# Kernel optimization log

Measured on AMD Instinct MI355X. Metric: run time of the kernel, lower is better.

The kernel has to match this reference:

```python
import jax, jax.numpy as jnp
import numpy as np

EPS = 1e-7
TWO_PI = 2.0 * np.pi

K = 4096   # num gaussians
R = 8192   # num rays
MAP_SIZE = 100


def setup_inputs() -> dict:
    key = jax.random.key(0)
    k1, k2, k3, k4, k5, k6 = jax.random.split(key, 6)
    pos_raw = jax.random.normal(k1, (K, 2), dtype=jnp.float32)            # pre-sigmoid positions
    conc_raw = jax.random.normal(k2, (K,), dtype=jnp.float32)             # pre-softplus concentration
    scale_raw = 0.1 * jax.random.normal(k3, (K, 2), dtype=jnp.float32)    # log-scales
    rot_raw = jax.random.uniform(k4, (K,), dtype=jnp.float32) * TWO_PI    # rotation angles
    p_rays = jax.random.uniform(k5, (R, 2), dtype=jnp.float32) * MAP_SIZE # ray origins in map coords
    u = jax.random.normal(k6, (R, 2), dtype=jnp.float32)
    u_rays = u / jnp.linalg.norm(u, axis=-1, keepdims=True)               # unit ray directions
    return {"pos_raw": pos_raw, "conc_raw": conc_raw, "scale_raw": scale_raw,
            "rot_raw": rot_raw, "p_rays": p_rays, "u_rays": u_rays,
            "map_size": MAP_SIZE}


def _forward(pos_raw, conc_raw, scale_raw, rot_raw, p_rays, u_rays, map_size):
    # --- per-gaussian activations (GasSplattingModel getters) ---
    pos = jax.nn.sigmoid(pos_raw) * map_size           # (K,2)
    conc = jax.nn.softplus(conc_raw)                   # (K,)
    scale = jnp.exp(scale_raw)                         # (K,2)
    d0 = 1.0 / (scale[:, 0] ** 2 + EPS)                # diag of S^2 inverse
    d1 = 1.0 / (scale[:, 1] ** 2 + EPS)
    c, s = jnp.cos(rot_raw), jnp.sin(rot_raw)
    # Sigma^{-1} = R diag(d0,d1) R^T with R = [[c,-s],[s,c]]  (symmetric 2x2)
    m00 = c * c * d0 + s * s * d1                      # (K,)
    m01 = c * s * (d0 - d1)
    m11 = s * s * d0 + c * c * d1
    M = jnp.stack([m00, m01, m11], axis=0)             # (3,K) quadratic-form coeffs

    u0, u1 = u_rays[:, 0], u_rays[:, 1]
    p0, p1 = p_rays[:, 0], p_rays[:, 1]

    # quadratic-form features per ray, contracted with M via GEMM -> (R,K)
    qu = jnp.stack([u0 * u0, 2.0 * u0 * u1, u1 * u1], axis=1)        # (R,3)
    qp = jnp.stack([p0 * p0, 2.0 * p0 * p1, p1 * p1], axis=1)        # (R,3)
    qup = jnp.stack([u0 * p0, u0 * p1 + u1 * p0, u1 * p1], axis=1)   # (R,3)
    a = qu @ M          # u^T S u      (R,K)
    pSp = qp @ M        # p^T S p      (R,K)
    uSp = qup @ M       # u^T S p      (R,K)

    # S @ mu per gaussian -> (2,K)
    Sm = jnp.stack([m00 * pos[:, 0] + m01 * pos[:, 1],
                    m01 * pos[:, 0] + m11 * pos[:, 1]], axis=0)
    uSm = u_rays @ Sm   # u^T S mu     (R,K)
    pSm = p_rays @ Sm   # p^T S mu     (R,K)
    mSm = pos[:, 0] * Sm[0] + pos[:, 1] * Sm[1]        # mu^T S mu (K,)

    b = uSp - uSm                                      # u^T S (p - mu)
    c0 = pSp - 2.0 * pSm + mSm[None, :]                # (p-mu)^T S (p-mu)

    # closed-form line integral of conc * exp(-0.5 (x-mu)^T S (x-mu)) along ray
    dens = conc[None, :] * jnp.sqrt(TWO_PI / a) * jnp.exp(-0.5 * (c0 - b * b / a))
    return jnp.sum(dens, axis=-1)                      # (R,)


def reference(pos_raw, conc_raw, scale_raw, rot_raw, p_rays, u_rays, map_size):
    return _forward(pos_raw, conc_raw, scale_raw, rot_raw, p_rays, u_rays, map_size)
```

## Files before the change

### kernel.cpp

```cpp
#include <hip/hip_runtime.h>
#include <hip/hip_bf16.h>

#define EPS 1e-07f

#define BLOCK   512
#define RPB     32
#define SLICE_G 1024
#define NGRP    (SLICE_G/4)
#define NW      (BLOCK/64)
#define PBLOCK  64

#define SQRT_HALF_LOG2E 0.84932180028801904f
#define LOG2_SQRT_2PI   1.32574806473616588f

typedef float v4f __attribute__((ext_vector_type(4)));

__global__ __launch_bounds__(PBLOCK) void precompute_gauss(
                                 const float* __restrict__ pos_raw,
                                 const float* __restrict__ conc_raw,
                                 const float* __restrict__ scale_raw,
                                 const float* __restrict__ rot_raw,
                                 const void*  __restrict__ map_size_p,
                                 float* __restrict__ gG,
                                 float* __restrict__ out,
                                 int K, int KPAD, int R)
{
    int k = blockIdx.x * blockDim.x + threadIdx.x;
    int nthreads = gridDim.x * blockDim.x;

    for (int i = k; i < R; i += nthreads) out[i] = 0.0f;

    if (k >= KPAD) return;

    const int q = k >> 2, e = k & 3;
    float* rec = gG + q * 24;

    if (k >= K) {
        rec[0  + e] = 1.0f;
        rec[4  + e] = 0.0f;
        rec[8  + e] = 1.0f;
        rec[12 + e] = -1e38f;
        rec[16 + e] = 0.0f;
        rec[20 + e] = 0.0f;
        return;
    }

    unsigned int msbits = *(const unsigned int*)map_size_p;
    float msf = __uint_as_float(msbits);
    const float ms = (msf >= 1e-3f && msf <= 1e9f) ? msf
                                                   : (float)(*(const int*)map_size_p);

    float pr0 = pos_raw[2*k],  pr1 = pos_raw[2*k+1];
    float pos0 = ms / (1.0f + __expf(-pr0));
    float pos1 = ms / (1.0f + __expf(-pr1));

    float cr = conc_raw[k];
    float conc = fmaxf(cr, 0.0f) + __logf(1.0f + __expf(-fabsf(cr)));

    float s0 = __expf(scale_raw[2*k]);
    float s1 = __expf(scale_raw[2*k+1]);
    float d0 = 1.0f / (s0*s0 + EPS);
    float d1 = 1.0f / (s1*s1 + EPS);

    float rot = rot_raw[k];
    float c = __cosf(rot), s = __sinf(rot);

    float m00 = c*c*d0 + s*s*d1;
    float m01 = c*s*(d0 - d1);
    float m11 = s*s*d0 + c*c*d1;

    float det    = d0 * d1;
    float invdet = 1.0f / det;
    float cc = __log2f(conc) + LOG2_SQRT_2PI - 0.5f * __log2f(det);

    rec[0  + e] = m00 * invdet;
    rec[4  + e] = m01 * invdet;
    rec[8  + e] = m11 * invdet;
    rec[12 + e] = cc;
    rec[16 + e] = pos0;
    rec[20 + e] = pos1;
}

__global__ __launch_bounds__(BLOCK) void splat_main(
        const float* __restrict__ p_rays,
        const float* __restrict__ u_rays,
        const float* __restrict__ gG,
        float* __restrict__ out,
        int R)
{
    __shared__ v4f  sG4[NGRP * 6];
    __shared__ float psum[NW][RPB];

    const int tid   = threadIdx.x;
    const int lane  = tid & 63;
    const int wv    = tid >> 6;
    const int rayl  = lane & 31;
    const int half  = lane >> 5;
    const int chunk = (wv << 1) | half;
    const int NG    = NGRP / 16;

    int ray = blockIdx.x * RPB + rayl;
    if (ray >= R) ray = R - 1;

    {
        const v4f* src = (const v4f*)(gG + (size_t)blockIdx.y * NGRP * 24);
        #pragma unroll
        for (int i = 0; i < (NGRP * 6) / BLOCK; ++i)
            sG4[tid + i * BLOCK] = src[tid + i * BLOCK];
    }

    float2 p2 = *(const float2*)(p_rays + 2*ray);
    float2 u2 = *(const float2*)(u_rays + 2*ray);
    const float p0 = p2.x, p1 = p2.y, u0 = u2.x, u1 = u2.y;
    const float qu0  = u0*u0, qu1 = 2.0f*u0*u1, qu2 = u1*u1;
    const float wt   =  SQRT_HALF_LOG2E * (u0*p1 - u1*p0);
    const float su1  =  SQRT_HALF_LOG2E * u1;
    const float nsu0 = -SQRT_HALF_LOG2E * u0;

    __syncthreads();

    float acc = 0.0f;
    const int g0 = chunk * NG;
    #pragma unroll 4
    for (int gq = 0; gq < NG; ++gq) {
        const v4f* g = &sG4[(g0 + gq) * 6];
        v4f M00 = g[0];
        v4f M01 = g[1];
        v4f M11 = g[2];
        v4f CC  = g[3];
        v4f P0  = g[4];
        v4f P1  = g[5];

        #pragma unroll
        for (int e = 0; e < 4; ++e) {
            float a_  = fmaf(qu2, M11[e], fmaf(qu1, M01[e], qu0 * M00[e]));
            float cr_ = fmaf(nsu0, P1[e], fmaf(su1, P0[e], wt));
            float ra_ = __builtin_amdgcn_rsqf(a_);
            float t_  = cr_ * ra_;
            float ar_ = fmaf(-t_, t_, CC[e]);
            float e_  = __builtin_amdgcn_exp2f(ar_);
            acc = fmaf(ra_, e_, acc);
        }
    }

    acc += __shfl_xor(acc, 32, 64);
    if (half == 0) psum[wv][rayl] = acc;
    __syncthreads();

    if (wv == 0 && lane < RPB) {
        float s = 0.0f;
        #pragma unroll
        for (int w = 0; w < NW; ++w) s += psum[w][lane];
        int oray = blockIdx.x * RPB + lane;
        if (oray < R) atomicAdd(&out[oray], s);
    }
}

extern "C" void kernel_launch(void* const* d_in, const int* in_sizes, int n_in,
                              void* d_out, int out_size, void* d_ws, size_t ws_size,
                              hipStream_t stream)
{
    const float* pos_raw   = (const float*)d_in[0];
    const float* conc_raw  = (const float*)d_in[1];
    const float* scale_raw = (const float*)d_in[2];
    const float* rot_raw   = (const float*)d_in[3];
    const float* p_rays    = (const float*)d_in[4];
    const float* u_rays    = (const float*)d_in[5];
    const void*  map_size  = d_in[6];

    const int K = in_sizes[1];
    const int R = out_size;

    const int NSLICE = (K + SLICE_G - 1) / SLICE_G;
    const int KPAD   = NSLICE * SLICE_G;

    float* out = (float*)d_out;
    float* gG  = (float*)d_ws;

    {
        dim3 grid((KPAD + PBLOCK - 1) / PBLOCK);
        precompute_gauss<<<grid, PBLOCK, 0, stream>>>(pos_raw, conc_raw, scale_raw,
                                                      rot_raw, map_size,
                                                      gG, out, K, KPAD, R);
    }
    {
        dim3 grid((R + RPB - 1) / RPB, NSLICE);
        splat_main<<<grid, BLOCK, 0, stream>>>(p_rays, u_rays, gG, out, R);
    }
}
```

Baseline: 21.65 us.

## Process two rays per thread and halve the gaussian slice size

Each thread now evaluates two rays against every gaussian loaded from shared memory, so each LDS read is reused twice, and blocks cover 64 rays. The gaussian slice per block shrinks from 1024 to 512, which doubles the slices along y and keeps the total block count the same. This also halves shared-memory use per block, and launch bounds now request 8 waves per SIMD. The costs are more register pressure, twice as many atomic adds to the output, and more redundant ray loads across slices.

Result: slower. 25.22 us (+16.5%).

```diff
diff --git a/kernel.cpp b/kernel.cpp
--- a/kernel.cpp
+++ b/kernel.cpp
@@ -4,9 +4,11 @@
 #define EPS 1e-07f
 
 #define BLOCK   512
-#define RPB     32
-#define SLICE_G 1024
+#define RPB     64
+#define SLICE_G 512
 #define NGRP    (SLICE_G/4)
+#define NCHUNK  16
+#define NG      (NGRP/NCHUNK)
 #define NW      (BLOCK/64)
 #define PBLOCK  64
 
@@ -81,7 +83,7 @@
     rec[20 + e] = pos1;
 }
 
-__global__ __launch_bounds__(BLOCK) void splat_main(
+__global__ __launch_bounds__(BLOCK, 8) void splat_main(
         const float* __restrict__ p_rays,
         const float* __restrict__ u_rays,
         const float* __restrict__ gG,
@@ -97,31 +99,39 @@
     const int rayl  = lane & 31;
     const int half  = lane >> 5;
     const int chunk = (wv << 1) | half;
-    const int NG    = NGRP / 16;
-
-    int ray = blockIdx.x * RPB + rayl;
-    if (ray >= R) ray = R - 1;
+
+    const int rbase = blockIdx.x * RPB;
+    int ray0 = rbase + rayl;
+    int ray1 = rbase + 32 + rayl;
+    if (ray0 >= R) ray0 = R - 1;
+    if (ray1 >= R) ray1 = R - 1;
 
     {
         const v4f* src = (const v4f*)(gG + (size_t)blockIdx.y * NGRP * 24);
-        #pragma unroll
-        for (int i = 0; i < (NGRP * 6) / BLOCK; ++i)
-            sG4[tid + i * BLOCK] = src[tid + i * BLOCK];
-    }
-
-    float2 p2 = *(const float2*)(p_rays + 2*ray);
-    float2 u2 = *(const float2*)(u_rays + 2*ray);
-    const float p0 = p2.x, p1 = p2.y, u0 = u2.x, u1 = u2.y;
-    const float qu0  = u0*u0, qu1 = 2.0f*u0*u1, qu2 = u1*u1;
-    const float wt   =  SQRT_HALF_LOG2E * (u0*p1 - u1*p0);
-    const float su1  =  SQRT_HALF_LOG2E * u1;
-    const float nsu0 = -SQRT_HALF_LOG2E * u0;
+        for (int i = tid; i < NGRP * 6; i += BLOCK)
+            sG4[i] = src[i];
+    }
+
+    float qu0[2], qu1[2], qu2[2], wt[2], su1[2], nsu0[2];
+    #pragma unroll
+    for (int r = 0; r < 2; ++r) {
+        int ray = r ? ray1 : ray0;
+        float2 p2 = *(const float2*)(p_rays + 2*ray);
+        float2 u2 = *(const float2*)(u_rays + 2*ray);
+        float p0 = p2.x, p1 = p2.y, u0 = u2.x, u1 = u2.y;
+        qu0[r]  = u0*u0;
+        qu1[r]  = 2.0f*u0*u1;
+        qu2[r]  = u1*u1;
+        wt[r]   =  SQRT_HALF_LOG2E * (u0*p1 - u1*p0);
+        su1[r]  =  SQRT_HALF_LOG2E * u1;
+        nsu0[r] = -SQRT_HALF_LOG2E * u0;
+    }
 
     __syncthreads();
 
-    float acc = 0.0f;
+    float acc0 = 0.0f, acc1 = 0.0f;
     const int g0 = chunk * NG;
-    #pragma unroll 4
+    #pragma unroll 2
     for (int gq = 0; gq < NG; ++gq) {
         const v4f* g = &sG4[(g0 + gq) * 6];
         v4f M00 = g[0];
@@ -133,25 +143,40 @@
 
         #pragma unroll
         for (int e = 0; e < 4; ++e) {
-            float a_  = fmaf(qu2, M11[e], fmaf(qu1, M01[e], qu0 * M00[e]));
-            float cr_ = fmaf(nsu0, P1[e], fmaf(su1, P0[e], wt));
-            float ra_ = __builtin_amdgcn_rsqf(a_);
-            float t_  = cr_ * ra_;
-            float ar_ = fmaf(-t_, t_, CC[e]);
-            float e_  = __builtin_amdgcn_exp2f(ar_);
-            acc = fmaf(ra_, e_, acc);
+            {
+                float a_  = fmaf(qu2[0], M11[e], fmaf(qu1[0], M01[e], qu0[0] * M00[e]));
+                float cr_ = fmaf(nsu0[0], P1[e], fmaf(su1[0], P0[e], wt[0]));
+                float ra_ = __builtin_amdgcn_rsqf(a_);
+                float t_  = cr_ * ra_;
+                float ar_ = fmaf(-t_, t_, CC[e]);
+                float e_  = __builtin_amdgcn_exp2f(ar_);
+                acc0 = fmaf(ra_, e_, acc0);
+            }
+            {
+                float a_  = fmaf(qu2[1], M11[e], fmaf(qu1[1], M01[e], qu0[1] * M00[e]));
+                float cr_ = fmaf(nsu0[1], P1[e], fmaf(su1[1], P0[e], wt[1]));
+                float ra_ = __builtin_amdgcn_rsqf(a_);
+                float t_  = cr_ * ra_;
+                float ar_ = fmaf(-t_, t_, CC[e]);
+                float e_  = __builtin_amdgcn_exp2f(ar_);
+                acc1 = fmaf(ra_, e_, acc1);
+            }
         }
     }
 
-    acc += __shfl_xor(acc, 32, 64);
-    if (half == 0) psum[wv][rayl] = acc;
+    acc0 += __shfl_xor(acc0, 32, 64);
+    acc1 += __shfl_xor(acc1, 32, 64);
+    if (half == 0) {
+        psum[wv][rayl]      = acc0;
+        psum[wv][rayl + 32] = acc1;
+    }
     __syncthreads();
 
-    if (wv == 0 && lane < RPB) {
+    if (wv == 0) {
         float s = 0.0f;
         #pragma unroll
         for (int w = 0; w < NW; ++w) s += psum[w][lane];
-        int oray = blockIdx.x * RPB + lane;
+        int oray = rbase + lane;
         if (oray < R) atomicAdd(&out[oray], s);
     }
 }
```
